# Optimization experiments

Hardware: AMD Instinct MI355X
Metric: run time of the kernel (lower is better)

Reference implementation:

```python
import jax, jax.numpy as jnp
import numpy as np

N = 16384
D = 128
TOPK = 32


def setup_inputs() -> dict:
    key = jax.random.key(0)
    kx, kw = jax.random.split(key)
    x = jax.random.normal(kx, (N,), dtype=jnp.float32)  # unused by the module's forward
    W = jax.random.normal(kw, (N, D), dtype=jnp.float32)  # embedding table (learned param)
    return {"x": x, "W": W}


def reference(x, W):
    # adj = E @ E^T : [N, N] similarity matrix
    adj = W @ W.T
    # per-row top-K (torch.topk along dim=1)
    vals, idx = jax.lax.top_k(adj, TOPK)  # [N, K] each
    # dense_to_sparse emits nonzeros in row-major order -> sort columns within each row.
    order = jnp.argsort(idx, axis=1)
    idx_s = jnp.take_along_axis(idx, order, axis=1)
    vals_s = jnp.take_along_axis(vals, order, axis=1)
    rows = jnp.repeat(jnp.arange(N, dtype=idx_s.dtype), TOPK)
    edge_index = jnp.stack([rows, idx_s.reshape(-1)])  # [2, N*K]
    edge_values = vals_s.reshape(-1)  # [N*K]
    return edge_index, edge_values
```

## Files before the change

kernel.cpp:

```cpp
#include <hip/hip_runtime.h>
#include <hip/hip_bf16.h>
#include <hip/hip_fp16.h>


#define N_ROWS 16384
#define DIM    128
#define TOPK   32
#define NK     (N_ROWS * TOPK)
#define ZTAU   2.45f
#define DELTA  0.05f
#define CAPL   192
#define WCAP   48
#define RPB    32
#define NWAVE  8
#define CPS    256
#define NSTG   (N_ROWS / CPS)
#define W1BIN  0.15625f
#define W2BIN  0.00244140625f

using short8   = __attribute__((ext_vector_type(8)))  short;
using floatx16 = __attribute__((ext_vector_type(16))) float;

#define PK_ROWS 32
__global__ __launch_bounds__(256)
void pack_kernel(const float* __restrict__ W, unsigned short* __restrict__ FA,
                 unsigned short* __restrict__ FB, float* __restrict__ norm) {
    __shared__ float lds[PK_ROWS * 132];
    __shared__ float nrmS[PK_ROWS];
    const int t  = threadIdx.x;
    const int rb = blockIdx.x * PK_ROWS;

    const float4* src = (const float4*)(W + (size_t)rb * DIM);
    #pragma unroll
    for (int i = 0; i < 4; ++i) {
        const int f = t + 256 * i;
        const float4 v = src[f];
        const int r = f >> 5, j = f & 31;
        *(float4*)&lds[r * 132 + j * 4] = v;
        float ss = v.x * v.x + v.y * v.y + v.z * v.z + v.w * v.w;
        #pragma unroll
        for (int off = 1; off < 32; off <<= 1) ss += __shfl_xor(ss, off, 64);
        if (j == 0) nrmS[r] = sqrtf(ss);
    }
    __syncthreads();

    const size_t blkoff = (size_t)blockIdx.x * 8192;
    unsigned* fa = (unsigned*)((char*)FA + blkoff);
    unsigned* fb = (unsigned*)((char*)FB + blkoff);
    #pragma unroll
    for (int i = 0; i < 8; ++i) {
        const int d   = t + 256 * i;
        const int q   = d >> 7, r31 = (d >> 2) & 31, w = d & 3;
        const float f0 = lds[r31 * 132 + q * 8 + w * 2];
        const float f1 = lds[r31 * 132 + q * 8 + w * 2 + 1];
        const float inv = 1.0f / nrmS[r31];
        __hip_bfloat16 b0 = __float2bfloat16(f0), b1 = __float2bfloat16(f1);
        fb[d] = (unsigned)(*(unsigned short*)&b0) | ((unsigned)(*(unsigned short*)&b1) << 16);
        __hip_bfloat16 a0 = __float2bfloat16(f0 * inv), a1 = __float2bfloat16(f1 * inv);
        fa[d] = (unsigned)(*(unsigned short*)&a0) | ((unsigned)(*(unsigned short*)&a1) << 16);
    }
    if (t < PK_ROWS) norm[rb + t] = nrmS[t];
}

__global__ __launch_bounds__(512, 4)
void fused_kernel(const unsigned short* __restrict__ FA,
                  const unsigned short* __restrict__ FB,
                  const float* __restrict__ W, const float* __restrict__ norm,
                  float* __restrict__ out) {
    __shared__ unsigned int scnt[RPB];
    __shared__ unsigned int candL[RPB * CAPL];
    __shared__ int          wcolS[NWAVE][WCAP];
    __shared__ double       dvalS[NWAVE][WCAP];
    __shared__ int          fcolS[NWAVE][TOPK];
    __shared__ float        fvalS[NWAVE][TOPK];
    __shared__ unsigned int wcntS[NWAVE], mcntS[NWAVE], fcntS[NWAVE];

    const int tid = threadIdx.x, lane = tid & 63, wid = tid >> 6;
    const int half = lane >> 5, l31 = lane & 31;
    const int rowbase = blockIdx.x * RPB;

    if (tid < RPB) scnt[tid] = 0u;
    __syncthreads();

    short8 afrag[8];
    {
        const char* ab = (const char*)FA + (size_t)(rowbase >> 5) * 8192
                       + half * 512 + l31 * 16;
        #pragma unroll
        for (int kt = 0; kt < 8; ++kt) afrag[kt] = *(const short8*)(ab + kt * 1024);
    }

    const int rbh = 4 * half;
    const char* bstream = (const char*)FB + (size_t)wid * 8192 + half * 512 + l31 * 16;

    for (int s = 0; s < NSTG; ++s) {
        const char* bp = bstream + (size_t)s * 65536;
        short8 bfr[8];
        #pragma unroll
        for (int kt = 0; kt < 8; ++kt) bfr[kt] = *(const short8*)(bp + kt * 1024);
        floatx16 acc = (floatx16)0.0f;
        #pragma unroll
        for (int kt = 0; kt < 8; ++kt)
            acc = __builtin_amdgcn_mfma_f32_32x32x16_bf16(afrag[kt], bfr[kt], acc, 0, 0, 0);
        const unsigned pcol = (unsigned)(s * CPS + wid * 32 + l31) << 16;
        #pragma unroll
        for (int r = 0; r < 16; ++r) {
            if (acc[r] > ZTAU) {
                const int rloc = rbh + (r & 3) + 8 * (r >> 2);
                unsigned slot = atomicAdd(&scnt[rloc], 1u);
                if (slot < CAPL)
                    candL[rloc * CAPL + slot] = pcol | __half_as_ushort(__float2half(acc[r]));
            }
        }
    }
    __syncthreads();

    unsigned int* histW = (unsigned int*)&dvalS[wid][0];
    for (int rr = 0; rr < 4; ++rr) {
        const int rloc = wid * 4 + rr;
        const int rowg = rowbase + rloc;
        int n = (int)scnt[rloc]; if (n > CAPL) n = CAPL;
        const unsigned int* cl = &candL[rloc * CAPL];

        if (lane == 0) { wcntS[wid] = 0u; mcntS[wid] = 0u; fcntS[wid] = 0u; }
        histW[lane] = 0u;
        for (int i = lane; i < n; i += 64) {
            const float v = __half2float(__ushort_as_half((unsigned short)(cl[i] & 0xFFFFu)));
            int b = (int)((v - ZTAU) * (1.0f / W1BIN));
            b = b < 0 ? 0 : (b > 63 ? 63 : b);
            atomicAdd(&histW[b], 1u);
        }
        unsigned sfx = histW[lane];
        #pragma unroll
        for (int off = 1; off < 64; off <<= 1) {
            unsigned u = __shfl_down(sfx, off, 64);
            if (lane + off < 64) sfx += u;
        }
        unsigned long long mk = __ballot(sfx >= (unsigned)TOPK);
        const int b1 = mk ? (63 - __clzll(mk)) : 0;
        unsigned Gup = __shfl(sfx, (b1 + 1) & 63, 64);
        if (b1 == 63) Gup = 0u;
        const float lo1 = ZTAU + (float)b1 * W1BIN;

        histW[lane] = 0u;
        for (int i = lane; i < n; i += 64) {
            const float v = __half2float(__ushort_as_half((unsigned short)(cl[i] & 0xFFFFu)));
            if (v >= lo1 && v < lo1 + W1BIN) {
                int b = (int)((v - lo1) * (1.0f / W2BIN));
                b = b < 0 ? 0 : (b > 63 ? 63 : b);
                atomicAdd(&histW[b], 1u);
            }
        }
        unsigned sfx2 = histW[lane];
        #pragma unroll
        for (int off = 1; off < 64; off <<= 1) {
            unsigned u = __shfl_down(sfx2, off, 64);
            if (lane + off < 64) sfx2 += u;
        }
        sfx2 += Gup;
        mk = __ballot(sfx2 >= (unsigned)TOPK);
        const int b2 = mk ? (63 - __clzll(mk)) : 0;
        const float vlo = lo1 + (float)b2 * W2BIN;
        const float vhi = vlo + W2BIN;

        for (int i = lane; i < n; i += 64) {
            const unsigned e = cl[i];
            const float v = __half2float(__ushort_as_half((unsigned short)(e & 0xFFFFu)));
            if (v > vhi + DELTA) {
                atomicAdd(&mcntS[wid], 1u);
            } else if (v >= vlo - DELTA) {
                unsigned u = atomicAdd(&wcntS[wid], 1u);
                if (u < WCAP) wcolS[wid][u] = (int)(e >> 16);
            }
        }
        const int m = (int)mcntS[wid];
        int wn = (int)wcntS[wid]; if (wn > WCAP) wn = WCAP;
        int need = TOPK - m; if (need < 0) need = 0;

        if (lane < wn) {
            const int col = wcolS[wid][lane] & (N_ROWS - 1);
            const float4* wa = (const float4*)(W + (size_t)rowg * DIM);
            const float4* wb = (const float4*)(W + (size_t)col * DIM);
            double d0 = 0, d1 = 0, d2 = 0, d3 = 0;
            #pragma unroll
            for (int k = 0; k < DIM / 4; ++k) {
                const float4 x = wa[k]; const float4 y = wb[k];
                d0 += (double)x.x * y.x; d1 += (double)x.y * y.y;
                d2 += (double)x.z * y.z; d3 += (double)x.w * y.w;
            }
            dvalS[wid][lane] = (d0 + d1) + (d2 + d3);
        }
        if (lane < wn) {
            const double dv = dvalS[wid][lane]; const int c = wcolS[wid][lane];
            int r = 0;
            for (int u = 0; u < wn; ++u) {
                const double du = dvalS[wid][u];
                r += (du > dv || (du == dv && wcolS[wid][u] < c)) ? 1 : 0;
            }
            if (r < need) {
                unsigned slot = atomicAdd(&fcntS[wid], 1u);
                if (slot < TOPK) { fcolS[wid][slot] = c; fvalS[wid][slot] = (float)dv; }
            }
        }
        const float nm = norm[rowg];
        for (int i = lane; i < n; i += 64) {
            const unsigned e = cl[i];
            const float v = __half2float(__ushort_as_half((unsigned short)(e & 0xFFFFu)));
            if (v > vhi + DELTA) {
                unsigned slot = atomicAdd(&fcntS[wid], 1u);
                if (slot < TOPK) { fcolS[wid][slot] = (int)(e >> 16); fvalS[wid][slot] = v * nm; }
            }
        }
        int fn = (int)fcntS[wid]; if (fn > TOPK) fn = TOPK;
        if (lane < fn) {
            const int c = fcolS[wid][lane];
            int pos = 0;
            for (int j = 0; j < fn; ++j) pos += (fcolS[wid][j] < c) ? 1 : 0;
            const size_t base = (size_t)rowg * TOPK + pos;
            out[base]                  = (float)rowg;
            out[NK + base]             = (float)c;
            out[2 * (size_t)NK + base] = fvalS[wid][lane];
        }
    }
}

extern "C" void kernel_launch(void* const* d_in, const int* in_sizes, int n_in,
                              void* d_out, int out_size, void* d_ws, size_t ws_size,
                              hipStream_t stream) {
    (void)in_sizes; (void)n_in; (void)out_size; (void)ws_size;
    const float* W   = (const float*)d_in[1];
    float*       out = (float*)d_out;

    char* ws = (char*)d_ws;
    unsigned short* FA   = (unsigned short*)ws;
    unsigned short* FB   = (unsigned short*)(ws + (size_t)4194304);
    float*          norm = (float*)(ws + (size_t)8388608);

    pack_kernel<<<N_ROWS / PK_ROWS, 256, 0, stream>>>(W, FA, FB, norm);
    fused_kernel<<<N_ROWS / RPB, 512, 0, stream>>>(FA, FB, W, norm, out);
}
```

Measured before the change: 226.1 us.

## Double-buffer B fragment loads, stagger stage order per block, vectorize pack stores

The main MFMA loop now prefetches the next stage's B fragments into a second register buffer while the current stage computes, so global load latency overlaps with the matrix ops. Each block starts at a different stage offset, so blocks do not all stream the same part of FB at once. The pack kernel now reads float4 from LDS and writes uint2, halving its loop trips. Candidate order within each row changes with the start stage, and the extra buffer adds register pressure at the 512-thread, 4-block launch bound.

```diff
diff --git a/kernel.cpp b/kernel.cpp
--- a/kernel.cpp
+++ b/kernel.cpp
@@ -45,19 +45,25 @@
     __syncthreads();
 
     const size_t blkoff = (size_t)blockIdx.x * 8192;
-    unsigned* fa = (unsigned*)((char*)FA + blkoff);
-    unsigned* fb = (unsigned*)((char*)FB + blkoff);
+    uint2* fa = (uint2*)((char*)FA + blkoff);
+    uint2* fb = (uint2*)((char*)FB + blkoff);
     #pragma unroll
-    for (int i = 0; i < 8; ++i) {
-        const int d   = t + 256 * i;
-        const int q   = d >> 7, r31 = (d >> 2) & 31, w = d & 3;
-        const float f0 = lds[r31 * 132 + q * 8 + w * 2];
-        const float f1 = lds[r31 * 132 + q * 8 + w * 2 + 1];
+    for (int i = 0; i < 4; ++i) {
+        const int p   = t + 256 * i;
+        const int D   = 2 * p;
+        const int q   = D >> 7, r31 = (D >> 2) & 31, w = D & 3;
+        const float4 f4 = *(const float4*)&lds[r31 * 132 + q * 8 + w * 2];
         const float inv = 1.0f / nrmS[r31];
-        __hip_bfloat16 b0 = __float2bfloat16(f0), b1 = __float2bfloat16(f1);
-        fb[d] = (unsigned)(*(unsigned short*)&b0) | ((unsigned)(*(unsigned short*)&b1) << 16);
-        __hip_bfloat16 a0 = __float2bfloat16(f0 * inv), a1 = __float2bfloat16(f1 * inv);
-        fa[d] = (unsigned)(*(unsigned short*)&a0) | ((unsigned)(*(unsigned short*)&a1) << 16);
+        __hip_bfloat16 b0 = __float2bfloat16(f4.x), b1 = __float2bfloat16(f4.y);
+        __hip_bfloat16 b2 = __float2bfloat16(f4.z), b3 = __float2bfloat16(f4.w);
+        fb[p] = make_uint2(
+            (unsigned)(*(unsigned short*)&b0) | ((unsigned)(*(unsigned short*)&b1) << 16),
+            (unsigned)(*(unsigned short*)&b2) | ((unsigned)(*(unsigned short*)&b3) << 16));
+        __hip_bfloat16 a0 = __float2bfloat16(f4.x * inv), a1 = __float2bfloat16(f4.y * inv);
+        __hip_bfloat16 a2 = __float2bfloat16(f4.z * inv), a3 = __float2bfloat16(f4.w * inv);
+        fa[p] = make_uint2(
+            (unsigned)(*(unsigned short*)&a0) | ((unsigned)(*(unsigned short*)&a1) << 16),
+            (unsigned)(*(unsigned short*)&a2) | ((unsigned)(*(unsigned short*)&a3) << 16));
     }
     if (t < PK_ROWS) norm[rb + t] = nrmS[t];
 }
@@ -92,12 +98,9 @@
 
     const int rbh = 4 * half;
     const char* bstream = (const char*)FB + (size_t)wid * 8192 + half * 512 + l31 * 16;
-
-    for (int s = 0; s < NSTG; ++s) {
-        const char* bp = bstream + (size_t)s * 65536;
-        short8 bfr[8];
-        #pragma unroll
-        for (int kt = 0; kt < 8; ++kt) bfr[kt] = *(const short8*)(bp + kt * 1024);
+    const int s0 = (blockIdx.x * 37) & (NSTG - 1);
+
+    auto step = [&](const short8* bfr, int s) {
         floatx16 acc = (floatx16)0.0f;
         #pragma unroll
         for (int kt = 0; kt < 8; ++kt)
@@ -112,6 +115,28 @@
                     candL[rloc * CAPL + slot] = pcol | __half_as_ushort(__float2half(acc[r]));
             }
         }
+    };
+
+    short8 bX[8], bY[8];
+    {
+        const char* bp = bstream + (size_t)s0 * 65536;
+        #pragma unroll
+        for (int kt = 0; kt < 8; ++kt) bX[kt] = *(const short8*)(bp + kt * 1024);
+    }
+    for (int i = 0; i < NSTG; i += 2) {
+        const int sA = (s0 + i) & (NSTG - 1);
+        const int sB = (s0 + i + 1) & (NSTG - 1);
+        const char* bp1 = bstream + (size_t)sB * 65536;
+        #pragma unroll
+        for (int kt = 0; kt < 8; ++kt) bY[kt] = *(const short8*)(bp1 + kt * 1024);
+        step(bX, sA);
+        if (i + 2 < NSTG) {
+            const int sC = (s0 + i + 2) & (NSTG - 1);
+            const char* bp2 = bstream + (size_t)sC * 65536;
+            #pragma unroll
+            for (int kt = 0; kt < 8; ++kt) bX[kt] = *(const short8*)(bp2 + kt * 1024);
+        }
+        step(bY, sB);
     }
     __syncthreads();
 
```

After: 284.9 us. 1.26x slower.

## Switch candidate-screening GEMM from bf16 to int8 MFMA with per-row scales

Applied to the files above, without the earlier changes.

Quantizes W rows to int8 using a per-row absmax scale and computes the screening similarity with i32_32x32x32_i8 MFMA, rescaling by per-row inverse factors to recover the cosine-normalized score. This halves the streamed B-operand bytes and uses the higher int8 MFMA rate. It also staggers the starting stage per block to spread L2/HBM access. The refinement margin DELTA and per-wave capacity are widened to absorb the larger quantization error, which risks more candidates and more refine work.

```diff
diff --git a/kernel.cpp b/kernel.cpp
--- a/kernel.cpp
+++ b/kernel.cpp
@@ -8,9 +8,9 @@
 #define TOPK   32
 #define NK     (N_ROWS * TOPK)
 #define ZTAU   2.45f
-#define DELTA  0.05f
+#define DELTA  0.14f
 #define CAPL   192
-#define WCAP   48
+#define WCAP   64
 #define RPB    32
 #define NWAVE  8
 #define CPS    256
@@ -18,53 +18,61 @@
 #define W1BIN  0.15625f
 #define W2BIN  0.00244140625f
 
-using short8   = __attribute__((ext_vector_type(8)))  short;
-using floatx16 = __attribute__((ext_vector_type(16))) float;
-
-#define PK_ROWS 32
+using int4v    = __attribute__((ext_vector_type(4)))  int;
+using intx16   = __attribute__((ext_vector_type(16))) int;
+
+#define PK_ROWS 64
 __global__ __launch_bounds__(256)
-void pack_kernel(const float* __restrict__ W, unsigned short* __restrict__ FA,
-                 unsigned short* __restrict__ FB, float* __restrict__ norm) {
+void pack_kernel(const float* __restrict__ W, signed char* __restrict__ FQ,
+                 float* __restrict__ invA, float* __restrict__ invB,
+                 float* __restrict__ norm) {
     __shared__ float lds[PK_ROWS * 132];
-    __shared__ float nrmS[PK_ROWS];
+    __shared__ float nrmS[PK_ROWS], amxS[PK_ROWS];
     const int t  = threadIdx.x;
     const int rb = blockIdx.x * PK_ROWS;
 
     const float4* src = (const float4*)(W + (size_t)rb * DIM);
     #pragma unroll
-    for (int i = 0; i < 4; ++i) {
+    for (int i = 0; i < 8; ++i) {
         const int f = t + 256 * i;
         const float4 v = src[f];
         const int r = f >> 5, j = f & 31;
         *(float4*)&lds[r * 132 + j * 4] = v;
         float ss = v.x * v.x + v.y * v.y + v.z * v.z + v.w * v.w;
-        #pragma unroll
-        for (int off = 1; off < 32; off <<= 1) ss += __shfl_xor(ss, off, 64);
-        if (j == 0) nrmS[r] = sqrtf(ss);
+        float am = fmaxf(fmaxf(fabsf(v.x), fabsf(v.y)), fmaxf(fabsf(v.z), fabsf(v.w)));
+        #pragma unroll
+        for (int off = 1; off < 32; off <<= 1) {
+            ss += __shfl_xor(ss, off, 64);
+            am = fmaxf(am, __shfl_xor(am, off, 64));
+        }
+        if (j == 0) { nrmS[r] = sqrtf(ss); amxS[r] = am; }
     }
     __syncthreads();
 
-    const size_t blkoff = (size_t)blockIdx.x * 8192;
-    unsigned* fa = (unsigned*)((char*)FA + blkoff);
-    unsigned* fb = (unsigned*)((char*)FB + blkoff);
+    unsigned* fq = (unsigned*)(FQ + (size_t)blockIdx.x * 8192);
     #pragma unroll
     for (int i = 0; i < 8; ++i) {
         const int d   = t + 256 * i;
-        const int q   = d >> 7, r31 = (d >> 2) & 31, w = d & 3;
-        const float f0 = lds[r31 * 132 + q * 8 + w * 2];
-        const float f1 = lds[r31 * 132 + q * 8 + w * 2 + 1];
-        const float inv = 1.0f / nrmS[r31];
-        __hip_bfloat16 b0 = __float2bfloat16(f0), b1 = __float2bfloat16(f1);
-        fb[d] = (unsigned)(*(unsigned short*)&b0) | ((unsigned)(*(unsigned short*)&b1) << 16);
-        __hip_bfloat16 a0 = __float2bfloat16(f0 * inv), a1 = __float2bfloat16(f1 * inv);
-        fa[d] = (unsigned)(*(unsigned short*)&a0) | ((unsigned)(*(unsigned short*)&a1) << 16);
-    }
-    if (t < PK_ROWS) norm[rb + t] = nrmS[t];
+        const int fb  = d >> 10, rem = d & 1023;
+        const int q   = rem >> 7, c31 = (rem >> 2) & 31, sub = rem & 3;
+        const int row = fb * 32 + c31;
+        const float4 v = *(const float4*)&lds[row * 132 + q * 16 + sub * 4];
+        const float sc = 126.0f / amxS[row];
+        const int q0 = (int)rintf(v.x * sc), q1 = (int)rintf(v.y * sc);
+        const int q2 = (int)rintf(v.z * sc), q3 = (int)rintf(v.w * sc);
+        fq[d] = (unsigned)(q0 & 255) | ((unsigned)(q1 & 255) << 8)
+              | ((unsigned)(q2 & 255) << 16) | ((unsigned)(q3 & 255) << 24);
+    }
+    if (t < PK_ROWS) {
+        norm[rb + t] = nrmS[t];
+        invA[rb + t] = amxS[t] / (126.0f * nrmS[t]);
+        invB[rb + t] = amxS[t] / 126.0f;
+    }
 }
 
 __global__ __launch_bounds__(512, 4)
-void fused_kernel(const unsigned short* __restrict__ FA,
-                  const unsigned short* __restrict__ FB,
+void fused_kernel(const signed char* __restrict__ FQ,
+                  const float* __restrict__ invA, const float* __restrict__ invB,
                   const float* __restrict__ W, const float* __restrict__ norm,
                   float* __restrict__ out) {
     __shared__ unsigned int scnt[RPB];
@@ -82,34 +90,43 @@
     if (tid < RPB) scnt[tid] = 0u;
     __syncthreads();
 
-    short8 afrag[8];
+    int4v afrag[4];
     {
-        const char* ab = (const char*)FA + (size_t)(rowbase >> 5) * 8192
+        const char* ab = (const char*)FQ + (size_t)(rowbase >> 5) * 4096
                        + half * 512 + l31 * 16;
         #pragma unroll
-        for (int kt = 0; kt < 8; ++kt) afrag[kt] = *(const short8*)(ab + kt * 1024);
-    }
-
+        for (int kt = 0; kt < 4; ++kt) afrag[kt] = *(const int4v*)(ab + kt * 1024);
+    }
     const int rbh = 4 * half;
-    const char* bstream = (const char*)FB + (size_t)wid * 8192 + half * 512 + l31 * 16;
-
-    for (int s = 0; s < NSTG; ++s) {
-        const char* bp = bstream + (size_t)s * 65536;
-        short8 bfr[8];
-        #pragma unroll
-        for (int kt = 0; kt < 8; ++kt) bfr[kt] = *(const short8*)(bp + kt * 1024);
-        floatx16 acc = (floatx16)0.0f;
-        #pragma unroll
-        for (int kt = 0; kt < 8; ++kt)
-            acc = __builtin_amdgcn_mfma_f32_32x32x16_bf16(afrag[kt], bfr[kt], acc, 0, 0, 0);
+    float invA16[16];
+    #pragma unroll
+    for (int r = 0; r < 16; ++r)
+        invA16[r] = invA[rowbase + rbh + (r & 3) + 8 * (r >> 2)];
+
+    const char* bstream = (const char*)FQ + (size_t)wid * 4096 + half * 512 + l31 * 16;
+    const int s0 = (37 * (blockIdx.x & 255)) & (NSTG - 1);
+
+    for (int i = 0; i < NSTG; ++i) {
+        const int s = (s0 + i) & (NSTG - 1);
+        const char* bp = bstream + (size_t)s * 32768;
+        const float invb = invB[s * CPS + wid * 32 + l31];
+        int4v bfr[4];
+        #pragma unroll
+        for (int kt = 0; kt < 4; ++kt) bfr[kt] = *(const int4v*)(bp + kt * 1024);
+        intx16 acc = (intx16)0;
+        #pragma unroll
+        for (int kt = 0; kt < 4; ++kt)
+            acc = __builtin_amdgcn_mfma_i32_32x32x32_i8(afrag[kt], bfr[kt], acc, 0, 0, 0);
+
         const unsigned pcol = (unsigned)(s * CPS + wid * 32 + l31) << 16;
         #pragma unroll
         for (int r = 0; r < 16; ++r) {
-            if (acc[r] > ZTAU) {
+            const float v = (float)acc[r] * invA16[r] * invb;
+            if (v > ZTAU) {
                 const int rloc = rbh + (r & 3) + 8 * (r >> 2);
                 unsigned slot = atomicAdd(&scnt[rloc], 1u);
                 if (slot < CAPL)
-                    candL[rloc * CAPL + slot] = pcol | __half_as_ushort(__float2half(acc[r]));
+                    candL[rloc * CAPL + slot] = pcol | __half_as_ushort(__float2half(v));
             }
         }
     }
@@ -232,10 +249,11 @@
     float*       out = (float*)d_out;
 
     char* ws = (char*)d_ws;
-    unsigned short* FA   = (unsigned short*)ws;
-    unsigned short* FB   = (unsigned short*)(ws + (size_t)4194304);
-    float*          norm = (float*)(ws + (size_t)8388608);
-
-    pack_kernel<<<N_ROWS / PK_ROWS, 256, 0, stream>>>(W, FA, FB, norm);
-    fused_kernel<<<N_ROWS / RPB, 512, 0, stream>>>(FA, FB, W, norm, out);
+    signed char* FQ   = (signed char*)ws;
+    float*       norm = (float*)(ws + (size_t)2097152);
+    float*       invA = (float*)(ws + (size_t)2162688);
+    float*       invB = (float*)(ws + (size_t)2228224);
+
+    pack_kernel<<<N_ROWS / PK_ROWS, 256, 0, stream>>>(W, FQ, invA, invB, norm);
+    fused_kernel<<<N_ROWS / RPB, 512, 0, stream>>>(FQ, invA, invB, W, norm, out);
 }
```

New measurement: 209.4 us. 7.4% less time.
